# Kernel optimization log

Measured on AMD Instinct MI355X. Metric: run time of the kernel, lower is better.

The kernel has to match this reference:

```python
import jax, jax.numpy as jnp
import numpy as np

K = 3
TOP_K = 10
MASK_RATIO = 0.5
EPS_COS = 1e-8
EPS_DEG = 1e-6


def setup_inputs() -> dict:
    key = jax.random.key(0)
    ks = jax.random.split(key, 10)
    N, C, H, O, E = 4096, 128, 128, 64, 65536
    x = jax.random.normal(ks[0], (N, C), dtype=jnp.float32)
    edge_index = jax.random.randint(ks[1], (2, E), 0, N, dtype=jnp.int64)
    alpha = jnp.full((K,), 1.0 / K, dtype=jnp.float32)
    fusion_W = 0.02 * jax.random.normal(ks[2], (2 * H, H), dtype=jnp.float32)
    fusion_b = jnp.zeros((H,), dtype=jnp.float32)
    lin0_W = 0.02 * jax.random.normal(ks[3], (C, H), dtype=jnp.float32)
    lin0_b = jnp.zeros((H,), dtype=jnp.float32)
    lin1_W = 0.02 * jax.random.normal(ks[4], (H, O), dtype=jnp.float32)
    lin1_b = jnp.zeros((O,), dtype=jnp.float32)
    return {
        "x": x, "edge_index": edge_index, "alpha": alpha,
        "fusion_W": fusion_W, "fusion_b": fusion_b,
        "lin0_W": lin0_W, "lin0_b": lin0_b,
        "lin1_W": lin1_W, "lin1_b": lin1_b,
    }


def reference(x, edge_index, alpha, fusion_W, fusion_b, lin0_W, lin0_b, lin1_W, lin1_b):
    N = x.shape[0]
    # dense adjacency and its powers: A^0 = I (so A^0 @ x = x), A^1, A^2
    A = jnp.zeros((N, N), x.dtype).at[edge_index[0], edge_index[1]].set(1.0)
    A2 = A @ A
    hop_feats = jnp.stack([x, A @ x, A2 @ x], axis=0)  # [K, N, C]

    # per-node cosine-similarity top-k (self always included, cos=1)
    xn = x / (jnp.linalg.norm(x, axis=-1, keepdims=True) + EPS_COS)
    sim = xn @ xn.T  # [N, N]
    _, topk_idx = jax.lax.top_k(sim, TOP_K)  # [N, TOP_K]

    # random keep-mask per node, forced True at top-k neighbors
    mask = jax.random.uniform(jax.random.key(42), (N, N)) < MASK_RATIO
    rows = jnp.arange(N)[:, None]
    mask = mask.at[rows, topk_idx].set(True)
    Mf = mask.astype(x.dtype)  # [N, N]

    # alpha-weighted multi-hop aggregate, masked mean over selected nodes
    agg = jnp.einsum('k,knc->nc', alpha, hop_feats)  # [N, C]
    fused = (Mf @ agg) / (Mf.sum(axis=1, keepdims=True) + EPS_DEG)  # [N, C]

    h = jnp.concatenate([x, fused], axis=-1) @ fusion_W + fusion_b
    h = jax.nn.relu(h @ lin0_W + lin0_b)  # dropout inactive in eval
    out = h @ lin1_W + lin1_b
    return jax.nn.log_softmax(out, axis=1)
```

## Files before the change

### kernel.cpp

```cpp
#include <hip/hip_runtime.h>
#include <hip/hip_bf16.h>
#include <stdint.h>


#define N_NODES 4096
#define C_DIM   128
#define WPR     128
#define HALF_P  8388608u
#define TOPK    10
#define JSPLIT  4

typedef __attribute__((ext_vector_type(8))) short bf16x8;
typedef __attribute__((ext_vector_type(4))) float f32x4;

__device__ __forceinline__ uint16_t f2bf(float f) {
    uint32_t u = __float_as_uint(f);
    return (uint16_t)((u + 0x7FFFu + ((u >> 16) & 1u)) >> 16);
}

__device__ __forceinline__ uint32_t rotl32(uint32_t v, int r) {
    return (v << r) | (v >> (32 - r));
}

__device__ __forceinline__ void threefry2x32(uint32_t k0, uint32_t k1,
                                             uint32_t x0, uint32_t x1,
                                             uint32_t& o0, uint32_t& o1) {
    uint32_t ks2 = k0 ^ k1 ^ 0x1BD11BDAu;
    x0 += k0; x1 += k1;
#define TF_ROUND(r) { x0 += x1; x1 = rotl32(x1, (r)); x1 ^= x0; }
    TF_ROUND(13) TF_ROUND(15) TF_ROUND(26) TF_ROUND(6)
    x0 += k1;  x1 += ks2 + 1u;
    TF_ROUND(17) TF_ROUND(29) TF_ROUND(16) TF_ROUND(24)
    x0 += ks2; x1 += k0 + 2u;
    TF_ROUND(13) TF_ROUND(15) TF_ROUND(26) TF_ROUND(6)
    x0 += k0;  x1 += k1 + 3u;
    TF_ROUND(17) TF_ROUND(29) TF_ROUND(16) TF_ROUND(24)
    x0 += k1;  x1 += ks2 + 4u;
    TF_ROUND(13) TF_ROUND(15) TF_ROUND(26) TF_ROUND(6)
    x0 += ks2; x1 += k0 + 5u;
#undef TF_ROUND
    o0 = x0; o1 = x1;
}

__global__ void detect_kernel(const uint32_t* __restrict__ ew,
                              uint32_t* __restrict__ flags) {
    __shared__ int cnt_oddnz;
    int t = threadIdx.x;
    if (t == 0) cnt_oddnz = 0;
    __syncthreads();
    if (ew[2 * t + 1] != 0u) atomicAdd(&cnt_oddnz, 1);
    __syncthreads();
    if (t == 0) flags[0] = (cnt_oddnz > 8) ? 0u : 1u;
}

__global__ void scatter_kernel(const int* __restrict__ ei, int E,
                               uint32_t* __restrict__ Abits,
                               const uint32_t* __restrict__ flags) {
    int e = blockIdx.x * blockDim.x + threadIdx.x;
    if (e >= E) return;
    int src, dst;
    if (flags[0]) { src = ei[2 * e]; dst = ei[2 * (E + e)]; }
    else          { src = ei[e];     dst = ei[E + e]; }
    src &= (N_NODES - 1);
    dst &= (N_NODES - 1);
    atomicOr(&Abits[src * WPR + (dst >> 5)], 1u << (dst & 31));
}

__global__ void spmm_kernel(const uint32_t* __restrict__ Abits,
                            const float* __restrict__ in,
                            float* __restrict__ out) {
    int i = blockIdx.x;
    int c = threadIdx.x;
    __shared__ uint32_t wbits[WPR];
    wbits[c] = Abits[i * WPR + c];
    __syncthreads();
    float acc = 0.f;
    for (int w = 0; w < WPR; ++w) {
        uint32_t bits = wbits[w];
        while (bits) {
            int b = __ffs(bits) - 1;
            bits &= bits - 1;
            acc += in[(w * 32 + b) * C_DIM + c];
        }
    }
    out[i * C_DIM + c] = acc;
}

__global__ void spmm2_agg_kernel(const uint32_t* __restrict__ Abits,
                                 const float* __restrict__ hop1,
                                 const float* __restrict__ xf,
                                 const float* __restrict__ alpha,
                                 float* __restrict__ agg) {
    int i = blockIdx.x;
    int c = threadIdx.x;
    __shared__ uint32_t wbits[WPR];
    wbits[c] = Abits[i * WPR + c];
    __syncthreads();
    float acc = 0.f;
    for (int w = 0; w < WPR; ++w) {
        uint32_t bits = wbits[w];
        while (bits) {
            int b = __ffs(bits) - 1;
            bits &= bits - 1;
            acc += hop1[(w * 32 + b) * C_DIM + c];
        }
    }
    agg[i * C_DIM + c] = alpha[0] * xf[i * C_DIM + c]
                       + alpha[1] * hop1[i * C_DIM + c]
                       + alpha[2] * acc;
}

__global__ void norm_kernel(const float* __restrict__ xf,
                            uint16_t* __restrict__ xnb) {
    int i = blockIdx.x;
    int c = threadIdx.x;
    float v = xf[i * C_DIM + c];
    float sq = v * v;
    #pragma unroll
    for (int off = 32; off >= 1; off >>= 1) sq += __shfl_xor(sq, off);
    __shared__ float ws[2];
    if ((c & 63) == 0) ws[c >> 6] = sq;
    __syncthreads();
    float tot = ws[0] + ws[1];
    xnb[i * C_DIM + c] = f2bf(v / (sqrtf(tot) + 1e-8f));
}

__global__ void transpose_bf_kernel(const float* __restrict__ agg,
                                    uint16_t* __restrict__ aggTb) {
    __shared__ float tile[32][33];
    int bi = blockIdx.x;
    int bc = blockIdx.y;
    int tx = threadIdx.x & 31, ty = threadIdx.x >> 5;
    #pragma unroll
    for (int r = 0; r < 32; r += 8)
        tile[ty + r][tx] = agg[(size_t)(bi * 32 + ty + r) * C_DIM + bc * 32 + tx];
    __syncthreads();
    #pragma unroll
    for (int r = 0; r < 32; r += 8)
        aggTb[(size_t)(bc * 32 + ty + r) * N_NODES + bi * 32 + tx] =
            f2bf(tile[tx][ty + r]);
}

__global__ void mask_kernel(uint32_t* __restrict__ Mbits) {
    uint32_t tid = blockIdx.x * blockDim.x + threadIdx.x;
    uint32_t base = tid * 32u;
    uint32_t w0 = 0u, w1 = 0u;
    for (int k = 0; k < 32; ++k) {
        uint32_t o0, o1;
        threefry2x32(0u, 42u, base + k, HALF_P + base + k, o0, o1);
        w0 |= (uint32_t)((o0 >> 31) ^ 1u) << k;
        w1 |= (uint32_t)((o1 >> 31) ^ 1u) << k;
    }
    Mbits[tid] = w0;
    Mbits[(HALF_P >> 5) + tid] = w1;
}

__launch_bounds__(512, 4)
__global__ void topk_kernel(const uint16_t* __restrict__ xnb,
                            float* __restrict__ topv,
                            int* __restrict__ topi) {
    int i0 = blockIdx.x * 16;
    int part = blockIdx.y;
    int t = threadIdx.x;
    int w = t >> 6;
    int lane = t & 63;
    int col = lane & 15;
    int quad = lane >> 4;

    __shared__ float sval[16 * 32 * TOPK];
    __shared__ int   sidx[16 * 32 * TOPK];

    bf16x8 bfi[4];
    #pragma unroll
    for (int s = 0; s < 4; ++s)
        bfi[s] = *(const bf16x8*)&xnb[(size_t)(i0 + col) * C_DIM + s * 32 + quad * 8];

    float tv[TOPK]; int ti[TOPK];
    #pragma unroll
    for (int k = 0; k < TOPK; ++k) { tv[k] = -1e30f; ti[k] = 0x7fffffff; }

    int jt0 = part * 64 + w * 8;
    for (int p = 0; p < 8; ++p) {
        int j0 = (jt0 + p) * 16;
        f32x4 acc = {0.f, 0.f, 0.f, 0.f};
        #pragma unroll
        for (int s = 0; s < 4; ++s) {
            bf16x8 aj = *(const bf16x8*)&xnb[(size_t)(j0 + col) * C_DIM + s * 32 + quad * 8];
            acc = __builtin_amdgcn_mfma_f32_16x16x32_bf16(aj, bfi[s], acc, 0, 0, 0);
        }
        float m4 = fmaxf(fmaxf(acc[0], acc[1]), fmaxf(acc[2], acc[3]));
        if (m4 > tv[TOPK-1]) {
            #pragma unroll
            for (int r = 0; r < 4; ++r) {
                float d = acc[r];
                if (d > tv[TOPK-1]) {
                    int j = j0 + quad * 4 + r;
                    tv[TOPK-1] = d; ti[TOPK-1] = j;
                    #pragma unroll
                    for (int q = TOPK - 2; q >= 0; --q) {
                        if (tv[q+1] > tv[q]) {
                            float fv = tv[q]; tv[q] = tv[q+1]; tv[q+1] = fv;
                            int iv = ti[q];  ti[q] = ti[q+1];  ti[q+1] = iv;
                        }
                    }
                }
            }
        }
    }

    int base = (col * 32 + w * 4 + quad) * TOPK;
    #pragma unroll
    for (int k = 0; k < TOPK; ++k) { sval[base + k] = tv[k]; sidx[base + k] = ti[k]; }

    int row = t >> 5, L = t & 31;
    for (int s = 16; s >= 1; s >>= 1) {
        __syncthreads();
        if (L < s) {
            int la = (row * 32 + L) * TOPK;
            int lb = (row * 32 + L + s) * TOPK;
            float ov[TOPK]; int oi[TOPK];
            int ia = 0, ib = 0;
            #pragma unroll
            for (int k = 0; k < TOPK; ++k) {
                float va = sval[la + ia], vb = sval[lb + ib];
                int   xa = sidx[la + ia], xb = sidx[lb + ib];
                bool takeA = (va > vb) || (va == vb && xa < xb);
                if (takeA) { ov[k] = va; oi[k] = xa; ++ia; }
                else       { ov[k] = vb; oi[k] = xb; ++ib; }
            }
            #pragma unroll
            for (int k = 0; k < TOPK; ++k) { sval[la + k] = ov[k]; sidx[la + k] = oi[k]; }
        }
    }
    __syncthreads();
    if (t < 16) {
        size_t gi = (size_t)(part * N_NODES + i0 + t) * TOPK;
        #pragma unroll
        for (int k = 0; k < TOPK; ++k) {
            topv[gi + k] = sval[(t * 32) * TOPK + k];
            topi[gi + k] = sidx[(t * 32) * TOPK + k];
        }
    }
}

__global__ void topmerge_kernel(const float* __restrict__ topv,
                                const int* __restrict__ topi,
                                uint32_t* __restrict__ Mbits) {
    int i = blockIdx.x * blockDim.x + threadIdx.x;
    if (i >= N_NODES) return;
    const float* v[JSPLIT]; const int* x[JSPLIT]; int ix[JSPLIT];
    #pragma unroll
    for (int q = 0; q < JSPLIT; ++q) {
        v[q] = topv + (size_t)(q * N_NODES + i) * TOPK;
        x[q] = topi + (size_t)(q * N_NODES + i) * TOPK;
        ix[q] = 0;
    }
    #pragma unroll
    for (int k = 0; k < TOPK; ++k) {
        float bestv = -1e38f; int bestj = 0x7fffffff; int bestq = 0;
        #pragma unroll
        for (int q = 0; q < JSPLIT; ++q) {
            bool ok = ix[q] < TOPK;
            float fv = ok ? v[q][ix[q]] : -1e38f;
            int   jj = ok ? x[q][ix[q]] : 0x7fffffff;
            if (fv > bestv || (fv == bestv && jj < bestj)) {
                bestv = fv; bestj = jj; bestq = q;
            }
        }
        ++ix[bestq];
        Mbits[(size_t)i * WPR + (bestj >> 5)] |= 1u << (bestj & 31);
    }
}

__global__ void deg_kernel(const uint32_t* __restrict__ Mbits,
                           float* __restrict__ deg) {
    int i = blockIdx.x;
    int l = threadIdx.x;
    const uint32_t* row = Mbits + (size_t)i * WPR;
    int c = __popc(row[l]) + __popc(row[l + 64]);
    #pragma unroll
    for (int off = 32; off >= 1; off >>= 1) c += __shfl_xor(c, off);
    if (l == 0) deg[i] = (float)c;
}

__launch_bounds__(512, 2)
__global__ void fused_kernel(const uint32_t* __restrict__ Mbits,
                             const uint16_t* __restrict__ aggTb,
                             const float* __restrict__ deg,
                             float* __restrict__ fused) {
    int i0 = blockIdx.x * 16;
    int t = threadIdx.x;
    int w = t >> 6;
    int lane = t & 63;
    int col = lane & 15;
    int quad = lane >> 4;
    __shared__ float sinv[16];
    if (t < 16) sinv[t] = 1.f / (deg[i0 + t] + 1e-6f);
    __syncthreads();

    const uint32_t* mrow = Mbits + (size_t)(i0 + col) * WPR;
    const uint16_t* brow = aggTb + (size_t)(w * 16 + col) * N_NODES;
    f32x4 acc[4];
    #pragma unroll
    for (int u = 0; u < 4; ++u) acc[u] = (f32x4){0.f, 0.f, 0.f, 0.f};

    for (int k0 = 0; k0 < N_NODES; k0 += 128) {
        uint4 mw4 = *(const uint4*)&mrow[k0 >> 5];
        uint32_t mws[4] = {mw4.x, mw4.y, mw4.z, mw4.w};
        #pragma unroll
        for (int u = 0; u < 4; ++u) {
            uint32_t byte = (mws[u] >> (quad * 8)) & 0xFFu;
            union { uint32_t uu[4]; bf16x8 v; } a;
            #pragma unroll
            for (int pp = 0; pp < 4; ++pp) {
                uint32_t lo = (byte >> (2 * pp)) & 1u;
                uint32_t hi = (byte >> (2 * pp + 1)) & 1u;
                a.uu[pp] = (lo ? 0x3F80u : 0u) | (hi ? 0x3F800000u : 0u);
            }
            bf16x8 b = *(const bf16x8*)&brow[k0 + u * 32 + quad * 8];
            acc[u] = __builtin_amdgcn_mfma_f32_16x16x32_bf16(a.v, b, acc[u], 0, 0, 0);
        }
    }
    #pragma unroll
    for (int r = 0; r < 4; ++r) {
        int il = quad * 4 + r;
        float s = (acc[0][r] + acc[1][r]) + (acc[2][r] + acc[3][r]);
        fused[(size_t)(i0 + il) * C_DIM + w * 16 + col] = s * sinv[il];
    }
}

__global__ void fusion_gemm(const float* __restrict__ xf,
                            const float* __restrict__ fused,
                            const float* __restrict__ W,
                            const float* __restrict__ b,
                            float* __restrict__ h) {
    int i0 = blockIdx.x * 4;
    int o = threadIdx.x;
    __shared__ float lx[4][256];
    for (int r = o; r < 4 * 128; r += 128) {
        lx[r >> 7][r & 127]         = xf[(size_t)(i0 + (r >> 7)) * C_DIM + (r & 127)];
        lx[r >> 7][128 + (r & 127)] = fused[(size_t)(i0 + (r >> 7)) * C_DIM + (r & 127)];
    }
    __syncthreads();
    float acc[4];
    #pragma unroll
    for (int r = 0; r < 4; ++r) acc[r] = b[o];
    for (int k = 0; k < 256; ++k) {
        float wv = W[k * 128 + o];
        #pragma unroll
        for (int r = 0; r < 4; ++r) acc[r] = fmaf(lx[r][k], wv, acc[r]);
    }
    #pragma unroll
    for (int r = 0; r < 4; ++r) h[(size_t)(i0 + r) * 128 + o] = acc[r];
}

__global__ void lin0_gemm(const float* __restrict__ h,
                          const float* __restrict__ W,
                          const float* __restrict__ b,
                          float* __restrict__ h1) {
    int i0 = blockIdx.x * 4;
    int o = threadIdx.x;
    __shared__ float lx[4][128];
    for (int r = o; r < 4 * 128; r += 128)
        lx[r >> 7][r & 127] = h[(size_t)(i0 + (r >> 7)) * 128 + (r & 127)];
    __syncthreads();
    float acc[4];
    #pragma unroll
    for (int r = 0; r < 4; ++r) acc[r] = b[o];
    for (int k = 0; k < 128; ++k) {
        float wv = W[k * 128 + o];
        #pragma unroll
        for (int r = 0; r < 4; ++r) acc[r] = fmaf(lx[r][k], wv, acc[r]);
    }
    #pragma unroll
    for (int r = 0; r < 4; ++r)
        h1[(size_t)(i0 + r) * 128 + o] = fmaxf(acc[r], 0.f);
}

__global__ void lin1_lsm(const float* __restrict__ h1,
                         const float* __restrict__ W,
                         const float* __restrict__ b,
                         float* __restrict__ out) {
    int i0 = blockIdx.x * 4;
    int o = threadIdx.x;
    __shared__ float lx[4][128];
    for (int r = o; r < 4 * 128; r += 64)
        lx[r >> 7][r & 127] = h1[(size_t)(i0 + (r >> 7)) * 128 + (r & 127)];
    __syncthreads();
    float acc[4];
    #pragma unroll
    for (int r = 0; r < 4; ++r) acc[r] = b[o];
    for (int k = 0; k < 128; ++k) {
        float wv = W[k * 64 + o];
        #pragma unroll
        for (int r = 0; r < 4; ++r) acc[r] = fmaf(lx[r][k], wv, acc[r]);
    }
    #pragma unroll
    for (int r = 0; r < 4; ++r) {
        float m = acc[r];
        #pragma unroll
        for (int off = 32; off >= 1; off >>= 1) m = fmaxf(m, __shfl_xor(m, off));
        float e = expf(acc[r] - m);
        float s = e;
        #pragma unroll
        for (int off = 32; off >= 1; off >>= 1) s += __shfl_xor(s, off);
        out[(size_t)(i0 + r) * 64 + o] = acc[r] - m - logf(s);
    }
}

extern "C" void kernel_launch(void* const* d_in, const int* in_sizes, int n_in,
                              void* d_out, int out_size, void* d_ws, size_t ws_size,
                              hipStream_t stream) {
    const float* xf    = (const float*)d_in[0];
    const int*   ei    = (const int*)d_in[1];
    const float* alpha = (const float*)d_in[2];
    const float* fW    = (const float*)d_in[3];
    const float* fB    = (const float*)d_in[4];
    const float* l0W   = (const float*)d_in[5];
    const float* l0B   = (const float*)d_in[6];
    const float* l1W   = (const float*)d_in[7];
    const float* l1B   = (const float*)d_in[8];
    float* out = (float*)d_out;
    const int E  = in_sizes[1] / 2;
    const int NC = N_NODES * C_DIM;

    char* p = (char*)d_ws;
    uint32_t* flags = (uint32_t*)p; p += 256;
    const size_t SZ = (size_t)NC * 4;
    uint32_t* Abits = (uint32_t*)p; p += SZ;
    float*    hop1  = (float*)p;    p += SZ;
    float*    agg   = (float*)p;    p += SZ;
    uint32_t* Mbits = (uint32_t*)p; p += SZ;
    float*    fusd  = (float*)p;    p += SZ;
    float*    h     = (float*)p;    p += SZ;
    float*    h1    = (float*)p;    p += SZ;
    uint16_t* xnb   = (uint16_t*)p; p += SZ / 2;
    uint16_t* aggTb = (uint16_t*)p; p += SZ / 2;
    float*    deg   = (float*)p;    p += N_NODES * 4;
    float*    topv  = (float*)p;    p += (size_t)JSPLIT * N_NODES * TOPK * 4;
    int*      topi  = (int*)p;      p += (size_t)JSPLIT * N_NODES * TOPK * 4;

    hipMemsetAsync(Abits, 0, SZ, stream);
    detect_kernel<<<1, 256, 0, stream>>>((const uint32_t*)ei, flags);
    scatter_kernel<<<(E + 255) / 256, 256, 0, stream>>>(ei, E, Abits, flags);
    spmm_kernel<<<N_NODES, 128, 0, stream>>>(Abits, xf, hop1);
    spmm2_agg_kernel<<<N_NODES, 128, 0, stream>>>(Abits, hop1, xf, alpha, agg);
    norm_kernel<<<N_NODES, 128, 0, stream>>>(xf, xnb);
    transpose_bf_kernel<<<dim3(128, 4), 256, 0, stream>>>(agg, aggTb);
    mask_kernel<<<(HALF_P >> 5) / 256, 256, 0, stream>>>(Mbits);
    topk_kernel<<<dim3(N_NODES / 16, JSPLIT), 512, 0, stream>>>(xnb, topv, topi);
    topmerge_kernel<<<N_NODES / 256, 256, 0, stream>>>(topv, topi, Mbits);
    deg_kernel<<<N_NODES, 64, 0, stream>>>(Mbits, deg);
    fused_kernel<<<N_NODES / 16, 512, 0, stream>>>(Mbits, aggTb, deg, fusd);
    fusion_gemm<<<N_NODES / 4, 128, 0, stream>>>(xf, fusd, fW, fB, h);
    lin0_gemm<<<N_NODES / 4, 128, 0, stream>>>(h, l0W, l0B, h1);
    lin1_lsm<<<N_NODES / 4, 64, 0, stream>>>(h1, l1W, l1B, out);
}
```

Baseline: 268.9 us.

## Fuse MLP stages, compute degree in mask kernel, split fused GEMM over K

Folds the dtype-detection kernel into scatter, computes per-row mask popcounts inside mask_kernel and updates them in topmerge, which removes deg_kernel. The fused masked-mean GEMM now splits K into two halves across a second grid dimension, writing partial sums that the new single MLP kernel combines. That kernel chains fusion, lin0 and lin1 with log-softmax, avoiding intermediate global writes and two launches. The topk kernel processes two MFMA tiles per iteration, pads its shared-memory stride to 11 and lowers its occupancy hint. The cost is atomics in mask_kernel and an extra partial-sum buffer read.

```diff
diff --git a/kernel.cpp b/kernel.cpp
--- a/kernel.cpp
+++ b/kernel.cpp
@@ -8,6 +8,7 @@
 #define WPR     128
 #define HALF_P  8388608u
 #define TOPK    10
+#define LSTR    11
 #define JSPLIT  4
 
 typedef __attribute__((ext_vector_type(8))) short bf16x8;
@@ -42,25 +43,20 @@
     o0 = x0; o1 = x1;
 }
 
-__global__ void detect_kernel(const uint32_t* __restrict__ ew,
-                              uint32_t* __restrict__ flags) {
+__global__ void scatter_kernel(const int* __restrict__ ei, int E,
+                               uint32_t* __restrict__ Abits) {
     __shared__ int cnt_oddnz;
     int t = threadIdx.x;
     if (t == 0) cnt_oddnz = 0;
     __syncthreads();
-    if (ew[2 * t + 1] != 0u) atomicAdd(&cnt_oddnz, 1);
-    __syncthreads();
-    if (t == 0) flags[0] = (cnt_oddnz > 8) ? 0u : 1u;
-}
-
-__global__ void scatter_kernel(const int* __restrict__ ei, int E,
-                               uint32_t* __restrict__ Abits,
-                               const uint32_t* __restrict__ flags) {
-    int e = blockIdx.x * blockDim.x + threadIdx.x;
+    if (((const uint32_t*)ei)[2 * t + 1] != 0u) atomicAdd(&cnt_oddnz, 1);
+    __syncthreads();
+    bool is64 = (cnt_oddnz <= 8);
+    int e = blockIdx.x * blockDim.x + t;
     if (e >= E) return;
     int src, dst;
-    if (flags[0]) { src = ei[2 * e]; dst = ei[2 * (E + e)]; }
-    else          { src = ei[e];     dst = ei[E + e]; }
+    if (is64) { src = ei[2 * e]; dst = ei[2 * (E + e)]; }
+    else      { src = ei[e];     dst = ei[E + e]; }
     src &= (N_NODES - 1);
     dst &= (N_NODES - 1);
     atomicOr(&Abits[src * WPR + (dst >> 5)], 1u << (dst & 31));
@@ -141,7 +137,8 @@
             f2bf(tile[tx][ty + r]);
 }
 
-__global__ void mask_kernel(uint32_t* __restrict__ Mbits) {
+__global__ void mask_kernel(uint32_t* __restrict__ Mbits,
+                            int* __restrict__ degpre) {
     uint32_t tid = blockIdx.x * blockDim.x + threadIdx.x;
     uint32_t base = tid * 32u;
     uint32_t w0 = 0u, w1 = 0u;
@@ -153,9 +150,20 @@
     }
     Mbits[tid] = w0;
     Mbits[(HALF_P >> 5) + tid] = w1;
-}
-
-__launch_bounds__(512, 4)
+    int p0 = __popc(w0), p1 = __popc(w1);
+    #pragma unroll
+    for (int off = 32; off >= 1; off >>= 1) {
+        p0 += __shfl_xor(p0, off);
+        p1 += __shfl_xor(p1, off);
+    }
+    if ((threadIdx.x & 63) == 0) {
+        int row0 = (int)(tid >> 7);
+        atomicAdd(&degpre[row0], p0);
+        atomicAdd(&degpre[2048 + row0], p1);
+    }
+}
+
+__launch_bounds__(512, 3)
 __global__ void topk_kernel(const uint16_t* __restrict__ xnb,
                             float* __restrict__ topv,
                             int* __restrict__ topi) {
@@ -167,8 +175,8 @@
     int col = lane & 15;
     int quad = lane >> 4;
 
-    __shared__ float sval[16 * 32 * TOPK];
-    __shared__ int   sidx[16 * 32 * TOPK];
+    __shared__ float sval[16 * 32 * LSTR];
+    __shared__ int   sidx[16 * 32 * LSTR];
 
     bf16x8 bfi[4];
     #pragma unroll
@@ -180,27 +188,36 @@
     for (int k = 0; k < TOPK; ++k) { tv[k] = -1e30f; ti[k] = 0x7fffffff; }
 
     int jt0 = part * 64 + w * 8;
-    for (int p = 0; p < 8; ++p) {
-        int j0 = (jt0 + p) * 16;
-        f32x4 acc = {0.f, 0.f, 0.f, 0.f};
+    for (int p = 0; p < 4; ++p) {
+        int j0a = (jt0 + 2 * p) * 16;
+        int j0b = j0a + 16;
+        f32x4 acc0 = {0.f, 0.f, 0.f, 0.f};
+        f32x4 acc1 = {0.f, 0.f, 0.f, 0.f};
         #pragma unroll
         for (int s = 0; s < 4; ++s) {
-            bf16x8 aj = *(const bf16x8*)&xnb[(size_t)(j0 + col) * C_DIM + s * 32 + quad * 8];
-            acc = __builtin_amdgcn_mfma_f32_16x16x32_bf16(aj, bfi[s], acc, 0, 0, 0);
-        }
-        float m4 = fmaxf(fmaxf(acc[0], acc[1]), fmaxf(acc[2], acc[3]));
-        if (m4 > tv[TOPK-1]) {
-            #pragma unroll
-            for (int r = 0; r < 4; ++r) {
-                float d = acc[r];
-                if (d > tv[TOPK-1]) {
-                    int j = j0 + quad * 4 + r;
-                    tv[TOPK-1] = d; ti[TOPK-1] = j;
-                    #pragma unroll
-                    for (int q = TOPK - 2; q >= 0; --q) {
-                        if (tv[q+1] > tv[q]) {
-                            float fv = tv[q]; tv[q] = tv[q+1]; tv[q+1] = fv;
-                            int iv = ti[q];  ti[q] = ti[q+1];  ti[q+1] = iv;
+            bf16x8 aj0 = *(const bf16x8*)&xnb[(size_t)(j0a + col) * C_DIM + s * 32 + quad * 8];
+            bf16x8 aj1 = *(const bf16x8*)&xnb[(size_t)(j0b + col) * C_DIM + s * 32 + quad * 8];
+            acc0 = __builtin_amdgcn_mfma_f32_16x16x32_bf16(aj0, bfi[s], acc0, 0, 0, 0);
+            acc1 = __builtin_amdgcn_mfma_f32_16x16x32_bf16(aj1, bfi[s], acc1, 0, 0, 0);
+        }
+        #pragma unroll
+        for (int g = 0; g < 2; ++g) {
+            f32x4 acc = g ? acc1 : acc0;
+            int j0 = g ? j0b : j0a;
+            float m4 = fmaxf(fmaxf(acc[0], acc[1]), fmaxf(acc[2], acc[3]));
+            if (m4 > tv[TOPK-1]) {
+                #pragma unroll
+                for (int r = 0; r < 4; ++r) {
+                    float d = acc[r];
+                    if (d > tv[TOPK-1]) {
+                        int j = j0 + quad * 4 + r;
+                        tv[TOPK-1] = d; ti[TOPK-1] = j;
+                        #pragma unroll
+                        for (int q = TOPK - 2; q >= 0; --q) {
+                            if (tv[q+1] > tv[q]) {
+                                float fv = tv[q]; tv[q] = tv[q+1]; tv[q+1] = fv;
+                                int iv = ti[q];  ti[q] = ti[q+1];  ti[q+1] = iv;
+                            }
                         }
                     }
                 }
@@ -208,7 +225,7 @@
         }
     }
 
-    int base = (col * 32 + w * 4 + quad) * TOPK;
+    int base = (col * 32 + w * 4 + quad) * LSTR;
     #pragma unroll
     for (int k = 0; k < TOPK; ++k) { sval[base + k] = tv[k]; sidx[base + k] = ti[k]; }
 
@@ -216,8 +233,8 @@
     for (int s = 16; s >= 1; s >>= 1) {
         __syncthreads();
         if (L < s) {
-            int la = (row * 32 + L) * TOPK;
-            int lb = (row * 32 + L + s) * TOPK;
+            int la = (row * 32 + L) * LSTR;
+            int lb = (row * 32 + L + s) * LSTR;
             float ov[TOPK]; int oi[TOPK];
             int ia = 0, ib = 0;
             #pragma unroll
@@ -237,15 +254,17 @@
         size_t gi = (size_t)(part * N_NODES + i0 + t) * TOPK;
         #pragma unroll
         for (int k = 0; k < TOPK; ++k) {
-            topv[gi + k] = sval[(t * 32) * TOPK + k];
-            topi[gi + k] = sidx[(t * 32) * TOPK + k];
+            topv[gi + k] = sval[(t * 32) * LSTR + k];
+            topi[gi + k] = sidx[(t * 32) * LSTR + k];
         }
     }
 }
 
 __global__ void topmerge_kernel(const float* __restrict__ topv,
                                 const int* __restrict__ topi,
-                                uint32_t* __restrict__ Mbits) {
+                                const int* __restrict__ degpre,
+                                uint32_t* __restrict__ Mbits,
+                                float* __restrict__ deg) {
     int i = blockIdx.x * blockDim.x + threadIdx.x;
     if (i >= N_NODES) return;
     const float* v[JSPLIT]; const int* x[JSPLIT]; int ix[JSPLIT];
@@ -255,6 +274,7 @@
         x[q] = topi + (size_t)(q * N_NODES + i) * TOPK;
         ix[q] = 0;
     }
+    int newc = 0;
     #pragma unroll
     for (int k = 0; k < TOPK; ++k) {
         float bestv = -1e38f; int bestj = 0x7fffffff; int bestq = 0;
@@ -268,35 +288,25 @@
             }
         }
         ++ix[bestq];
-        Mbits[(size_t)i * WPR + (bestj >> 5)] |= 1u << (bestj & 31);
-    }
-}
-
-__global__ void deg_kernel(const uint32_t* __restrict__ Mbits,
-                           float* __restrict__ deg) {
-    int i = blockIdx.x;
-    int l = threadIdx.x;
-    const uint32_t* row = Mbits + (size_t)i * WPR;
-    int c = __popc(row[l]) + __popc(row[l + 64]);
-    #pragma unroll
-    for (int off = 32; off >= 1; off >>= 1) c += __shfl_xor(c, off);
-    if (l == 0) deg[i] = (float)c;
+        uint32_t* wp = &Mbits[(size_t)i * WPR + (bestj >> 5)];
+        uint32_t old = *wp, bit = 1u << (bestj & 31);
+        newc += ((old & bit) == 0u);
+        *wp = old | bit;
+    }
+    deg[i] = (float)(degpre[i] + newc);
 }
 
 __launch_bounds__(512, 2)
 __global__ void fused_kernel(const uint32_t* __restrict__ Mbits,
                              const uint16_t* __restrict__ aggTb,
-                             const float* __restrict__ deg,
-                             float* __restrict__ fused) {
+                             float* __restrict__ fpart) {
     int i0 = blockIdx.x * 16;
+    int part = blockIdx.y;
     int t = threadIdx.x;
     int w = t >> 6;
     int lane = t & 63;
     int col = lane & 15;
     int quad = lane >> 4;
-    __shared__ float sinv[16];
-    if (t < 16) sinv[t] = 1.f / (deg[i0 + t] + 1e-6f);
-    __syncthreads();
 
     const uint32_t* mrow = Mbits + (size_t)(i0 + col) * WPR;
     const uint16_t* brow = aggTb + (size_t)(w * 16 + col) * N_NODES;
@@ -304,7 +314,8 @@
     #pragma unroll
     for (int u = 0; u < 4; ++u) acc[u] = (f32x4){0.f, 0.f, 0.f, 0.f};
 
-    for (int k0 = 0; k0 < N_NODES; k0 += 128) {
+    int kbase = part * 2048;
+    for (int k0 = kbase; k0 < kbase + 2048; k0 += 128) {
         uint4 mw4 = *(const uint4*)&mrow[k0 >> 5];
         uint32_t mws[4] = {mw4.x, mw4.y, mw4.z, mw4.w};
         #pragma unroll
@@ -325,86 +336,68 @@
     for (int r = 0; r < 4; ++r) {
         int il = quad * 4 + r;
         float s = (acc[0][r] + acc[1][r]) + (acc[2][r] + acc[3][r]);
-        fused[(size_t)(i0 + il) * C_DIM + w * 16 + col] = s * sinv[il];
-    }
-}
-
-__global__ void fusion_gemm(const float* __restrict__ xf,
-                            const float* __restrict__ fused,
-                            const float* __restrict__ W,
-                            const float* __restrict__ b,
-                            float* __restrict__ h) {
+        fpart[(size_t)part * (N_NODES * C_DIM)
+              + (size_t)(i0 + il) * C_DIM + w * 16 + col] = s;
+    }
+}
+
+__global__ void mlp_kernel(const float* __restrict__ xf,
+                           const float* __restrict__ fpart,
+                           const float* __restrict__ deg,
+                           const float* __restrict__ fW, const float* __restrict__ fB,
+                           const float* __restrict__ l0W, const float* __restrict__ l0B,
+                           const float* __restrict__ l1W, const float* __restrict__ l1B,
+                           float* __restrict__ out) {
     int i0 = blockIdx.x * 4;
-    int o = threadIdx.x;
+    int t = threadIdx.x;
     __shared__ float lx[4][256];
-    for (int r = o; r < 4 * 128; r += 128) {
-        lx[r >> 7][r & 127]         = xf[(size_t)(i0 + (r >> 7)) * C_DIM + (r & 127)];
-        lx[r >> 7][128 + (r & 127)] = fused[(size_t)(i0 + (r >> 7)) * C_DIM + (r & 127)];
+    __shared__ float hb[4][128];
+    const float* f0 = fpart;
+    const float* f1 = fpart + (size_t)N_NODES * C_DIM;
+    for (int r = t; r < 4 * 128; r += 128) {
+        int row = r >> 7, c = r & 127;
+        size_t idx = (size_t)(i0 + row) * C_DIM + c;
+        lx[row][c] = xf[idx];
+        lx[row][128 + c] = (f0[idx] + f1[idx]) / (deg[i0 + row] + 1e-6f);
     }
     __syncthreads();
     float acc[4];
     #pragma unroll
-    for (int r = 0; r < 4; ++r) acc[r] = b[o];
+    for (int r = 0; r < 4; ++r) acc[r] = fB[t];
     for (int k = 0; k < 256; ++k) {
-        float wv = W[k * 128 + o];
+        float wv = fW[k * 128 + t];
         #pragma unroll
         for (int r = 0; r < 4; ++r) acc[r] = fmaf(lx[r][k], wv, acc[r]);
     }
     #pragma unroll
-    for (int r = 0; r < 4; ++r) h[(size_t)(i0 + r) * 128 + o] = acc[r];
-}
-
-__global__ void lin0_gemm(const float* __restrict__ h,
-                          const float* __restrict__ W,
-                          const float* __restrict__ b,
-                          float* __restrict__ h1) {
-    int i0 = blockIdx.x * 4;
-    int o = threadIdx.x;
-    __shared__ float lx[4][128];
-    for (int r = o; r < 4 * 128; r += 128)
-        lx[r >> 7][r & 127] = h[(size_t)(i0 + (r >> 7)) * 128 + (r & 127)];
-    __syncthreads();
-    float acc[4];
-    #pragma unroll
-    for (int r = 0; r < 4; ++r) acc[r] = b[o];
+    for (int r = 0; r < 4; ++r) hb[r][t] = acc[r];
+    __syncthreads();
+    #pragma unroll
+    for (int r = 0; r < 4; ++r) acc[r] = l0B[t];
     for (int k = 0; k < 128; ++k) {
-        float wv = W[k * 128 + o];
-        #pragma unroll
-        for (int r = 0; r < 4; ++r) acc[r] = fmaf(lx[r][k], wv, acc[r]);
-    }
-    #pragma unroll
-    for (int r = 0; r < 4; ++r)
-        h1[(size_t)(i0 + r) * 128 + o] = fmaxf(acc[r], 0.f);
-}
-
-__global__ void lin1_lsm(const float* __restrict__ h1,
-                         const float* __restrict__ W,
-                         const float* __restrict__ b,
-                         float* __restrict__ out) {
-    int i0 = blockIdx.x * 4;
-    int o = threadIdx.x;
-    __shared__ float lx[4][128];
-    for (int r = o; r < 4 * 128; r += 64)
-        lx[r >> 7][r & 127] = h1[(size_t)(i0 + (r >> 7)) * 128 + (r & 127)];
-    __syncthreads();
-    float acc[4];
-    #pragma unroll
-    for (int r = 0; r < 4; ++r) acc[r] = b[o];
-    for (int k = 0; k < 128; ++k) {
-        float wv = W[k * 64 + o];
-        #pragma unroll
-        for (int r = 0; r < 4; ++r) acc[r] = fmaf(lx[r][k], wv, acc[r]);
-    }
-    #pragma unroll
-    for (int r = 0; r < 4; ++r) {
-        float m = acc[r];
+        float wv = l0W[k * 128 + t];
+        #pragma unroll
+        for (int r = 0; r < 4; ++r) acc[r] = fmaf(hb[r][k], wv, acc[r]);
+    }
+    __syncthreads();
+    #pragma unroll
+    for (int r = 0; r < 4; ++r) lx[r][t] = fmaxf(acc[r], 0.f);
+    __syncthreads();
+    int o = t & 63, pr = t >> 6;
+    #pragma unroll
+    for (int rr = 0; rr < 2; ++rr) {
+        int r = pr + 2 * rr;
+        float a = l1B[o];
+        for (int k = 0; k < 128; ++k)
+            a = fmaf(lx[r][k], l1W[k * 64 + o], a);
+        float m = a;
         #pragma unroll
         for (int off = 32; off >= 1; off >>= 1) m = fmaxf(m, __shfl_xor(m, off));
-        float e = expf(acc[r] - m);
+        float e = expf(a - m);
         float s = e;
         #pragma unroll
         for (int off = 32; off >= 1; off >>= 1) s += __shfl_xor(s, off);
-        out[(size_t)(i0 + r) * 64 + o] = acc[r] - m - logf(s);
+        out[(size_t)(i0 + r) * 64 + o] = a - m - logf(s);
     }
 }
 
@@ -425,34 +418,29 @@
     const int NC = N_NODES * C_DIM;
 
     char* p = (char*)d_ws;
-    uint32_t* flags = (uint32_t*)p; p += 256;
     const size_t SZ = (size_t)NC * 4;
-    uint32_t* Abits = (uint32_t*)p; p += SZ;
-    float*    hop1  = (float*)p;    p += SZ;
-    float*    agg   = (float*)p;    p += SZ;
-    uint32_t* Mbits = (uint32_t*)p; p += SZ;
-    float*    fusd  = (float*)p;    p += SZ;
-    float*    h     = (float*)p;    p += SZ;
-    float*    h1    = (float*)p;    p += SZ;
-    uint16_t* xnb   = (uint16_t*)p; p += SZ / 2;
-    uint16_t* aggTb = (uint16_t*)p; p += SZ / 2;
-    float*    deg   = (float*)p;    p += N_NODES * 4;
-    float*    topv  = (float*)p;    p += (size_t)JSPLIT * N_NODES * TOPK * 4;
-    int*      topi  = (int*)p;      p += (size_t)JSPLIT * N_NODES * TOPK * 4;
-
-    hipMemsetAsync(Abits, 0, SZ, stream);
-    detect_kernel<<<1, 256, 0, stream>>>((const uint32_t*)ei, flags);
-    scatter_kernel<<<(E + 255) / 256, 256, 0, stream>>>(ei, E, Abits, flags);
+    uint32_t* Abits  = (uint32_t*)p; p += SZ;
+    int*      degpre = (int*)p;      p += N_NODES * 4;
+    float*    hop1   = (float*)p;    p += SZ;
+    float*    agg    = (float*)p;    p += SZ;
+    uint32_t* Mbits  = (uint32_t*)p; p += SZ;
+    float*    fpart  = (float*)p;    p += 2 * SZ;
+    uint16_t* xnb    = (uint16_t*)p; p += SZ / 2;
+    uint16_t* aggTb  = (uint16_t*)p; p += SZ / 2;
+    float*    deg    = (float*)p;    p += N_NODES * 4;
+    float*    topv   = (float*)p;    p += (size_t)JSPLIT * N_NODES * TOPK * 4;
+    int*      topi   = (int*)p;      p += (size_t)JSPLIT * N_NODES * TOPK * 4;
+
+    hipMemsetAsync(Abits, 0, SZ + N_NODES * 4, stream);
+    scatter_kernel<<<(E + 255) / 256, 256, 0, stream>>>(ei, E, Abits);
     spmm_kernel<<<N_NODES, 128, 0, stream>>>(Abits, xf, hop1);
     spmm2_agg_kernel<<<N_NODES, 128, 0, stream>>>(Abits, hop1, xf, alpha, agg);
     norm_kernel<<<N_NODES, 128, 0, stream>>>(xf, xnb);
     transpose_bf_kernel<<<dim3(128, 4), 256, 0, stream>>>(agg, aggTb);
-    mask_kernel<<<(HALF_P >> 5) / 256, 256, 0, stream>>>(Mbits);
+    mask_kernel<<<(HALF_P >> 5) / 256, 256, 0, stream>>>(Mbits, degpre);
     topk_kernel<<<dim3(N_NODES / 16, JSPLIT), 512, 0, stream>>>(xnb, topv, topi);
-    topmerge_kernel<<<N_NODES / 256, 256, 0, stream>>>(topv, topi, Mbits);
-    deg_kernel<<<N_NODES, 64, 0, stream>>>(Mbits, deg);
-    fused_kernel<<<N_NODES / 16, 512, 0, stream>>>(Mbits, aggTb, deg, fusd);
-    fusion_gemm<<<N_NODES / 4, 128, 0, stream>>>(xf, fusd, fW, fB, h);
-    lin0_gemm<<<N_NODES / 4, 128, 0, stream>>>(h, l0W, l0B, h1);
-    lin1_lsm<<<N_NODES / 4, 64, 0, stream>>>(h1, l1W, l1B, out);
-}
+    topmerge_kernel<<<N_NODES / 256, 256, 0, stream>>>(topv, topi, degpre, Mbits, deg);
+    fused_kernel<<<dim3(N_NODES / 16, 2), 512, 0, stream>>>(Mbits, aggTb, fpart);
+    mlp_kernel<<<N_NODES / 4, 128, 0, stream>>>(xf, fpart, deg,
+                                                fW, fB, l0W, l0B, l1W, l1B, out);
+}
```

Measured after the change: 257.5 us. 1.04x faster.
